# Optimization experiments

Measured on AMD Instinct MI355X. Metric: run time of the kernel, lower is better.

Reference implementation:

```python
import jax, jax.numpy as jnp
import numpy as np

N = 200000   # nodes
E = 3200000  # edges
G = 8192     # graphs
F_IN = 28    # one-hot node feature dim (dataset.num_node_features)
D = 50       # embed_dim
H = 16       # hidden_channels
C = 2        # num_classes


def setup_inputs() -> dict:
    key = jax.random.key(0)
    ks = jax.random.split(key, 12)
    x = jax.random.normal(ks[0], (N, F_IN), jnp.float32)
    row = jax.random.randint(ks[1], (E,), 0, N)   # source nodes (edge_index[0])
    col = jax.random.randint(ks[2], (E,), 0, N)   # target nodes (edge_index[1])
    edge_attr = jax.random.uniform(ks[3], (E,), jnp.float32)
    batch = jnp.sort(jax.random.randint(ks[4], (N,), 0, G))
    emb = jax.random.normal(ks[5], (F_IN, D), jnp.float32) * 0.1
    W1 = jax.random.normal(ks[6], (D, H), jnp.float32) * (1.0 / np.sqrt(D))
    b1 = jnp.zeros((H,), jnp.float32)
    W2 = jax.random.normal(ks[7], (H, H), jnp.float32) * (1.0 / np.sqrt(H))
    b2 = jnp.zeros((H,), jnp.float32)
    W3 = jax.random.normal(ks[8], (H, C), jnp.float32) * (1.0 / np.sqrt(H))
    b3 = jnp.zeros((C,), jnp.float32)
    return dict(x=x, row=row, col=col, edge_attr=edge_attr, batch=batch,
                emb=emb, W1=W1, b1=b1, W2=W2, b2=b2, W3=W3, b3=b3)


def gcn_conv(h, row, col, ew, W, b):
    """PyG GCNConv with normalize=True, add_self_loops=True (fill_value=1)."""
    # degree at target nodes, including self-loop weight 1
    deg = jax.ops.segment_sum(ew, col, num_segments=N) + 1.0
    dinv = jnp.where(deg > 0, deg ** -0.5, 0.0)
    hw = h @ W                                   # [N, out]
    norm = dinv[row] * ew * dinv[col]            # [E]
    agg = jax.ops.segment_sum(hw[row] * norm[:, None], col, num_segments=N)
    agg = agg + hw * (dinv * dinv)[:, None]      # self-loop contribution
    return agg + b


def reference(x, row, col, edge_attr, batch, emb, W1, b1, W2, b2, W3, b3):
    # x is one-hot-ish -> argmax -> embedding lookup
    h = emb[jnp.argmax(x, axis=1)]               # [N, D]
    h = jax.nn.relu(gcn_conv(h, row, col, edge_attr, W1, b1))
    # dropout is identity in eval mode
    h = jax.nn.relu(gcn_conv(h, row, col, edge_attr, W2, b2))
    h = gcn_conv(h, row, col, edge_attr, W3, b3)  # [N, C]
    # global mean pool over graphs
    sums = jax.ops.segment_sum(h, batch, num_segments=G)
    cnts = jax.ops.segment_sum(jnp.ones((N,), h.dtype), batch, num_segments=G)
    pooled = sums / jnp.maximum(cnts, 1.0)[:, None]  # [G, C]
    return jax.nn.softmax(pooled, axis=1)
```

## Files before the change

### kernel.cpp

```cpp
#include <hip/hip_runtime.h>
#include <hip/hip_fp16.h>

constexpr int Nn  = 200000;
constexpr int Ne  = 3200000;
constexpr int Ng  = 8192;
constexpr int FIN = 28;
constexpr int DE  = 50;
constexpr int HD  = 16;
constexpr int CD  = 2;

constexpr int NBIN   = (Nn + 255) >> 8;
constexpr int NBLK   = 512;
constexpr int CH     = Ne / NBLK;
constexpr int CSTR   = 800;
constexpr int LDSCAP = 4608;

__device__ __forceinline__ float dec_ea(unsigned u) {
  return ((float)(u & 16383u) + 0.5f) * (1.0f / 16384.0f);
}

__device__ __forceinline__ float2 dec8(unsigned short u) {
  __half lo = __ushort_as_half((unsigned short)((u & 0x00ffu) << 8));
  __half hi = __ushort_as_half((unsigned short)(u & 0xff00u));
  return make_float2(__half2float(lo), __half2float(hi));
}
__device__ __forceinline__ unsigned char enc8(float f) {
  unsigned short b = __half_as_ushort(__float2half(f));
  return (unsigned char)((unsigned short)(b + 0x0080u) >> 8);
}

static inline int nblocks(long long n, int bs = 256, int cap = 16384) {
  long long b = (n + bs - 1) / bs;
  return (int)(b < cap ? b : cap);
}

__global__ __launch_bounds__(256) void k_count(const int* __restrict__ col,
                                               int* __restrict__ counts,
                                               const float* __restrict__ emb,
                                               const float* __restrict__ W1,
                                               float* __restrict__ EW1) {
  if (blockIdx.x == NBLK) {
    int t = threadIdx.x;
    for (int u = t; u < FIN * HD; u += 256) {
      int i = u / HD, k = u % HD;
      float s = 0.0f;
      for (int j = 0; j < DE; ++j) s += emb[i * DE + j] * W1[j * HD + k];
      EW1[u] = s;
    }
    return;
  }
  __shared__ int c[NBIN];
  for (int i = threadIdx.x; i < NBIN; i += 256) c[i] = 0;
  __syncthreads();
  int lo = blockIdx.x * CH;
  for (int i = threadIdx.x; i < CH; i += 256) atomicAdd(&c[col[lo + i] >> 8], 1);
  __syncthreads();
  for (int i = threadIdx.x; i < NBIN; i += 256) counts[blockIdx.x * CSTR + i] = c[i];
}

__global__ __launch_bounds__(256) void k_argmax(const float* __restrict__ x,
                                                unsigned char* __restrict__ arg) {
  __shared__ float xs[256 * FIN];
  int b = blockIdx.x, t = threadIdx.x;
  int base = b << 8;
  int nval = min(256, Nn - base) * FIN;
  const float4* x4 = (const float4*)(x + (size_t)base * FIN);
  float4* s4 = (float4*)xs;
  int n4 = nval >> 2;
  for (int i = t; i < n4; i += 256) s4[i] = x4[i];
  __syncthreads();
  int node = base + t;
  if (node >= Nn) return;
  const float* xp = xs + t * FIN;
  int a = 0; float best = xp[0];
#pragma unroll
  for (int j = 1; j < FIN; ++j) { float v = xp[j]; if (v > best) { best = v; a = j; } }
  arg[node] = (unsigned char)a;
}

__global__ __launch_bounds__(512) void k_scan1b(int* __restrict__ counts,
                                                int* __restrict__ colTotal) {
  __shared__ int s[NBLK];
  int bin = blockIdx.x, t = threadIdx.x;
  int v = counts[t * CSTR + bin];
  s[t] = v;
  __syncthreads();
  for (int d = 1; d < NBLK; d <<= 1) {
    int x = (t >= d) ? s[t - d] : 0;
    __syncthreads();
    s[t] += x;
    __syncthreads();
  }
  counts[t * CSTR + bin] = s[t] - v;
  if (t == NBLK - 1) colTotal[bin] = s[t];
}

__global__ __launch_bounds__(1024) void k_scanBins(const int* __restrict__ colTotal,
                                                   int* __restrict__ binBase,
                                                   int* __restrict__ start,
                                                   float* __restrict__ zeroreg,
                                                   int nzero) {
  for (int i = threadIdx.x; i < nzero; i += 1024) zeroreg[i] = 0.0f;
  __shared__ int s[1024];
  int t = threadIdx.x;
  int v = (t < NBIN) ? colTotal[t] : 0;
  s[t] = v;
  __syncthreads();
  for (int d = 1; d < 1024; d <<= 1) {
    int x = (t >= d) ? s[t - d] : 0;
    __syncthreads();
    s[t] += x;
    __syncthreads();
  }
  if (t < NBIN) binBase[t] = s[t] - v;
  if (t == NBIN - 1) { binBase[NBIN] = s[t]; start[Nn] = s[t]; }
}

__global__ __launch_bounds__(256) void k_place(const int* __restrict__ row,
                                               const int* __restrict__ col,
                                               const float* __restrict__ ea,
                                               const int* __restrict__ counts,
                                               const int* __restrict__ colTotal,
                                               const int* __restrict__ binBase,
                                               unsigned long long* __restrict__ staged) {
  __shared__ unsigned long long stage[CH];
  __shared__ int lhist[NBIN];
  __shared__ int lcur[NBIN];
  __shared__ int gbase[NBIN];
  __shared__ int partial[256];
  int blk = blockIdx.x, t = threadIdx.x;
  int lo = blk * CH;
  for (int i = t; i < NBIN; i += 256) {
    int cur = counts[blk * CSTR + i];
    int nxt = (blk == NBLK - 1) ? colTotal[i] : counts[(blk + 1) * CSTR + i];
    lhist[i] = nxt - cur;
    lcur[i] = 0;
    gbase[i] = binBase[i] + cur;
  }
  __syncthreads();
  constexpr int CPT = (NBIN + 255) / 256;
  int b0 = t * CPT, s = 0;
#pragma unroll
  for (int j = 0; j < CPT; ++j) { int b = b0 + j; if (b < NBIN) s += lhist[b]; }
  partial[t] = s;
  __syncthreads();
  for (int d = 1; d < 256; d <<= 1) {
    int x = (t >= d) ? partial[t - d] : 0;
    __syncthreads();
    partial[t] += x;
    __syncthreads();
  }
  int run = partial[t] - s;
#pragma unroll
  for (int j = 0; j < CPT; ++j) {
    int b = b0 + j;
    if (b < NBIN) { int c = lhist[b]; lhist[b] = run; run += c; }
  }
  __syncthreads();
  for (int i = t; i < CH; i += 256) {
    int e = lo + i;
    int c = col[e], bin = c >> 8;
    unsigned q = (unsigned)__float2int_rd(ea[e] * 16384.0f);
    if (q > 16383u) q = 16383u;
    unsigned long long entry =
        ((unsigned long long)(unsigned)c << 32) | ((unsigned)row[e] << 14) | q;
    int pos = lhist[bin] + atomicAdd(&lcur[bin], 1);
    stage[pos] = entry;
  }
  __syncthreads();
  for (int i = t; i < CH; i += 256) {
    unsigned long long entry = stage[i];
    int bin = (int)(entry >> 40);
    staged[gbase[bin] + (i - lhist[bin])] = entry;
  }
}

__global__ __launch_bounds__(256) void k_finemb(const int* __restrict__ binBase,
                                                const unsigned long long* __restrict__ staged,
                                                const unsigned char* __restrict__ arg,
                                                const float* __restrict__ EW1,
                                                unsigned* __restrict__ csr,
                                                int* __restrict__ start,
                                                float* __restrict__ dinv,
                                                unsigned char* __restrict__ hws1) {
  __shared__ int ncnt[256];
  __shared__ int noff[256];
  __shared__ int ncur[256];
  __shared__ float sdeg[256];
  __shared__ unsigned outb[LDSCAP];
  int b = blockIdx.x, t = threadIdx.x;
  int lo = binBase[b];
  int cnt = binBase[b + 1] - lo;
  if (cnt > LDSCAP) cnt = LDSCAP;
  ncnt[t] = 0; ncur[t] = 0; sdeg[t] = 0.0f;
  __syncthreads();
  for (int i = t; i < cnt; i += 256) {
    unsigned long long p = staged[lo + i];
    int cl = (int)((p >> 32) & 255u);
    atomicAdd(&ncnt[cl], 1);
    atomicAdd(&sdeg[cl], dec_ea((unsigned)p));
  }
  __syncthreads();
  int v = ncnt[t];
  noff[t] = v;
  __syncthreads();
  for (int d = 1; d < 256; d <<= 1) {
    int xsh = (t >= d) ? noff[t - d] : 0;
    __syncthreads();
    noff[t] += xsh;
    __syncthreads();
  }
  int excl = noff[t] - v;
  __syncthreads();
  noff[t] = excl;
  __syncthreads();
  for (int i = t; i < cnt; i += 256) {
    unsigned long long p = staged[lo + i];
    int cl = (int)((p >> 32) & 255u);
    int idx = noff[cl] + atomicAdd(&ncur[cl], 1);
    outb[idx] = (unsigned)p;
  }
  __syncthreads();
  for (int i = t; i < cnt; i += 256) csr[lo + i] = outb[i];
  int node = (b << 8) + t;
  if (node >= Nn) return;
  start[node] = lo + noff[t];
  float di = rsqrtf(sdeg[t] + 1.0f);
  dinv[node] = di;
  const float* ep = EW1 + (int)arg[node] * HD;
#pragma unroll
  for (int k = 0; k < HD; ++k) hws1[((size_t)node << 4) + k] = enc8(ep[k] * di);
}

template <int OUTC>
__global__ __launch_bounds__(256) void k_conv(const int* __restrict__ start,
                                              const unsigned* __restrict__ csr,
                                              const unsigned short* __restrict__ f8,
                                              const float* __restrict__ dinv,
                                              const float* __restrict__ bias,
                                              const float* __restrict__ Wn,
                                              void* __restrict__ outw) {
  int lane = threadIdx.x & 63;
  int slot = lane >> 3;
  int p    = lane & 7;
  int k    = lane & 15;
  int nstep = gridDim.x * 4;
  for (int n = blockIdx.x * 4 + (threadIdx.x >> 6); n < Nn; n += nstep) {
    int lo = start[n], hi = start[n + 1];
    int j0 = lo + slot;
    bool e0 = j0 < hi, e1 = j0 + 8 < hi, e2 = j0 + 16 < hi;
    unsigned u0 = __builtin_nontemporal_load(csr + (e0 ? j0 : 0));
    unsigned u1 = __builtin_nontemporal_load(csr + (e1 ? j0 + 8 : 0));
    unsigned u2 = __builtin_nontemporal_load(csr + (e2 ? j0 + 16 : 0));
    float w0 = e0 ? dec_ea(u0) : 0.0f;
    float w1 = e1 ? dec_ea(u1) : 0.0f;
    float w2 = e2 ? dec_ea(u2) : 0.0f;
    float2 v0 = dec8(f8[((u0 >> 14) << 3) + p]);
    float2 v1 = dec8(f8[((u1 >> 14) << 3) + p]);
    float2 v2 = dec8(f8[((u2 >> 14) << 3) + p]);
    float ax = fmaf(v2.x, w2, fmaf(v1.x, w1, v0.x * w0));
    float ay = fmaf(v2.y, w2, fmaf(v1.y, w1, v0.y * w0));
    for (int j = j0 + 24; j < hi; j += 8) {
      unsigned u = __builtin_nontemporal_load(csr + j);
      float w = dec_ea(u);
      float2 v = dec8(f8[((u >> 14) << 3) + p]);
      ax = fmaf(v.x, w, ax);
      ay = fmaf(v.y, w, ay);
    }
#pragma unroll
    for (int d = 8; d < 64; d <<= 1) {
      ax += __shfl_xor(ax, d, 64);
      ay += __shfl_xor(ay, d, 64);
    }
    float di = dinv[n];
    float2 self = dec8(f8[((size_t)n << 3) + p]);
    float h0 = fmaxf(di * (ax + self.x) + bias[2 * p + 0], 0.0f);
    float h1 = fmaxf(di * (ay + self.y) + bias[2 * p + 1], 0.0f);
    float acc2 = 0.0f;
#pragma unroll
    for (int q = 0; q < 8; ++q) {
      float hj0 = __shfl(h0, q, 64);
      float hj1 = __shfl(h1, q, 64);
      acc2 = fmaf(hj0, Wn[(2 * q + 0) * OUTC + (OUTC == 16 ? k : (k & 1))], acc2);
      acc2 = fmaf(hj1, Wn[(2 * q + 1) * OUTC + (OUTC == 16 ? k : (k & 1))], acc2);
    }
    acc2 *= di;
    if (OUTC == 16) {
      if (lane < 16) ((unsigned char*)outw)[((size_t)n << 4) + k] = enc8(acc2);
    } else {
      if (lane < CD) ((__half*)outw)[(size_t)n * CD + k] = __float2half(acc2);
    }
  }
}

__global__ __launch_bounds__(256) void k_conv3pool(const int* __restrict__ start,
                                                   const unsigned* __restrict__ csr,
                                                   const __half* __restrict__ h3,
                                                   const float* __restrict__ dinv,
                                                   const float* __restrict__ b3,
                                                   const int* __restrict__ batch,
                                                   float* __restrict__ sums,
                                                   float* __restrict__ cnts) {
  const __half2* h2 = (const __half2*)h3;
  int lane = threadIdx.x & 63;
  int nsub = lane >> 3;
  int slot = lane & 7;
  int wid  = threadIdx.x >> 6;
  int nstep = gridDim.x * 32;
  for (int nb = (blockIdx.x * 4 + wid) * 8; nb < Nn; nb += nstep) {
    int n = nb + nsub;
    int nn = min(n, Nn - 1);
    int lo = start[nn], hi = start[nn + 1];
    int j0 = lo + slot;
    bool e0 = j0 < hi, e1 = j0 + 8 < hi, e2 = j0 + 16 < hi;
    unsigned u0 = __builtin_nontemporal_load(csr + (e0 ? j0 : 0));
    unsigned u1 = __builtin_nontemporal_load(csr + (e1 ? j0 + 8 : 0));
    unsigned u2 = __builtin_nontemporal_load(csr + (e2 ? j0 + 16 : 0));
    float w0 = e0 ? dec_ea(u0) : 0.0f;
    float w1 = e1 ? dec_ea(u1) : 0.0f;
    float w2 = e2 ? dec_ea(u2) : 0.0f;
    float2 v0 = __half22float2(h2[u0 >> 14]);
    float2 v1 = __half22float2(h2[u1 >> 14]);
    float2 v2 = __half22float2(h2[u2 >> 14]);
    float ax = fmaf(v2.x, w2, fmaf(v1.x, w1, v0.x * w0));
    float ay = fmaf(v2.y, w2, fmaf(v1.y, w1, v0.y * w0));
    for (int j = j0 + 24; j < hi; j += 8) {
      unsigned u = __builtin_nontemporal_load(csr + j);
      float w = dec_ea(u);
      float2 v = __half22float2(h2[u >> 14]);
      ax = fmaf(v.x, w, ax);
      ay = fmaf(v.y, w, ay);
    }
    ax += __shfl_xor(ax, 1, 64); ay += __shfl_xor(ay, 1, 64);
    ax += __shfl_xor(ax, 2, 64); ay += __shfl_xor(ay, 2, 64);
    ax += __shfl_xor(ax, 4, 64); ay += __shfl_xor(ay, 4, 64);
    if (slot == 0 && n < Nn) {
      float di = dinv[n];
      float2 self = __half22float2(h2[n]);
      float a0 = di * (ax + self.x) + b3[0];
      float a1 = di * (ay + self.y) + b3[1];
      int g = batch[n];
      atomicAdd(&sums[2 * g + 0], a0);
      atomicAdd(&sums[2 * g + 1], a1);
      atomicAdd(&cnts[g], 1.0f);
    }
  }
}

__global__ void k_softmax(const float* __restrict__ sums, const float* __restrict__ cnts,
                          float* __restrict__ out, int g) {
  int stride = gridDim.x * blockDim.x;
  for (int i = blockIdx.x * blockDim.x + threadIdx.x; i < g; i += stride) {
    float cnt = fmaxf(cnts[i], 1.0f);
    float c0 = sums[i * 2 + 0] / cnt;
    float c1 = sums[i * 2 + 1] / cnt;
    float m = fmaxf(c0, c1);
    float e0 = __expf(c0 - m), e1 = __expf(c1 - m);
    float inv = 1.0f / (e0 + e1);
    out[i * 2 + 0] = e0 * inv;
    out[i * 2 + 1] = e1 * inv;
  }
}

extern "C" void kernel_launch(void* const* d_in, const int* in_sizes, int n_in,
                              void* d_out, int out_size, void* d_ws, size_t ws_size,
                              hipStream_t stream) {
  const float* x   = (const float*)d_in[0];
  const int*   row = (const int*)d_in[1];
  const int*   col = (const int*)d_in[2];
  const float* ea  = (const float*)d_in[3];
  const int*   bat = (const int*)d_in[4];
  const float* emb = (const float*)d_in[5];
  const float* W1  = (const float*)d_in[6];
  const float* b1  = (const float*)d_in[7];
  const float* W2  = (const float*)d_in[8];
  const float* b2  = (const float*)d_in[9];
  const float* W3  = (const float*)d_in[10];
  const float* b3  = (const float*)d_in[11];
  float* out = (float*)d_out;

  float* ws = (float*)d_ws;
  size_t o = 0;
  float* sums    = ws + o; o += (size_t)Ng * CD;
  float* cnts    = ws + o; o += Ng;
  float* dinv    = ws + o; o += Nn;
  float* EW1     = ws + o; o += FIN * HD + 16;
  int*   counts  = (int*)(ws + o); o += (size_t)NBLK * CSTR;
  int*   colTot  = (int*)(ws + o); o += CSTR;
  int*   binBase = (int*)(ws + o); o += 1024;
  int*   startp  = (int*)(ws + o); o += Nn + 16;
  unsigned char* argb = (unsigned char*)(ws + o); o += Nn / 4 + 16;
  unsigned long long* staged = (unsigned long long*)(ws + o); o += (size_t)Ne * 2;
  unsigned* csr  = (unsigned*)(ws + o); o += (size_t)Ne;
  unsigned char* hws1 = (unsigned char*)(ws + o); o += (size_t)Nn * HD / 4;
  unsigned char* hws2 = (unsigned char*)(ws + o); o += (size_t)Nn * HD / 4;
  __half* hw3s   = (__half*)(ws + o); o += (size_t)Nn * CD / 2;
  (void)ws_size; (void)n_in; (void)in_sizes; (void)out_size;

  k_count<<<NBLK + 1, 256, 0, stream>>>(col, counts, emb, W1, EW1);
  k_argmax<<<NBIN, 256, 0, stream>>>(x, argb);
  k_scan1b<<<NBIN, NBLK, 0, stream>>>(counts, colTot);
  k_scanBins<<<1, 1024, 0, stream>>>(colTot, binBase, startp, sums, Ng * (CD + 1));
  k_place<<<NBLK, 256, 0, stream>>>(row, col, ea, counts, colTot, binBase, staged);
  k_finemb<<<NBIN, 256, 0, stream>>>(binBase, staged, argb, EW1, csr, startp, dinv, hws1);

  k_conv<16><<<nblocks((long long)Nn * 64), 256, 0, stream>>>(
      startp, csr, (const unsigned short*)hws1, dinv, b1, W2, hws2);
  k_conv<2><<<nblocks((long long)Nn * 64), 256, 0, stream>>>(
      startp, csr, (const unsigned short*)hws2, dinv, b2, W3, hw3s);

  k_conv3pool<<<nblocks((long long)Nn * 8), 256, 0, stream>>>(
      startp, csr, hw3s, dinv, b3, bat, sums, cnts);

  k_softmax<<<nblocks(Ng), 256, 0, stream>>>(sums, cnts, out, Ng);
}
```

Baseline: 406.3 us.

## Replace global count/scan CSR build with fixed-capacity bins and atomic cursors

Drops the separate count, two scan kernels and the second read of col by giving each 256-node bin a fixed-capacity slab and claiming space with a global atomic cursor per bin in the placement kernel. Node degrees are stored as a separate array so that convs compute hi from start plus degree. Argmax, EW1 and zeroing are merged into one prep kernel, and the pool kernel reduces across the wavefront before doing atomics when all eight nodes share a graph. Edges past the bin capacity are silently dropped, and the CSR order within a bin now depends on atomic ordering.

```diff
diff --git a/kernel.cpp b/kernel.cpp
--- a/kernel.cpp
+++ b/kernel.cpp
@@ -9,11 +9,10 @@
 constexpr int HD  = 16;
 constexpr int CD  = 2;
 
-constexpr int NBIN   = (Nn + 255) >> 8;
-constexpr int NBLK   = 512;
-constexpr int CH     = Ne / NBLK;
-constexpr int CSTR   = 800;
-constexpr int LDSCAP = 4608;
+constexpr int NBIN = (Nn + 255) >> 8;
+constexpr int NBLK = 512;
+constexpr int CH   = Ne / NBLK;
+constexpr int CAPB = 4608;
 
 __device__ __forceinline__ float dec_ea(unsigned u) {
   return ((float)(u & 16383u) + 0.5f) * (1.0f / 16384.0f);
@@ -34,13 +33,14 @@
   return (int)(b < cap ? b : cap);
 }
 
-__global__ __launch_bounds__(256) void k_count(const int* __restrict__ col,
-                                               int* __restrict__ counts,
-                                               const float* __restrict__ emb,
-                                               const float* __restrict__ W1,
-                                               float* __restrict__ EW1) {
-  if (blockIdx.x == NBLK) {
-    int t = threadIdx.x;
+__global__ __launch_bounds__(256) void k_pre(const float* __restrict__ x,
+                                             unsigned char* __restrict__ arg,
+                                             const float* __restrict__ emb,
+                                             const float* __restrict__ W1,
+                                             float* __restrict__ EW1,
+                                             float* __restrict__ zreg, int nz) {
+  int b = blockIdx.x, t = threadIdx.x;
+  if (b == NBIN) {
     for (int u = t; u < FIN * HD; u += 256) {
       int i = u / HD, k = u % HD;
       float s = 0.0f;
@@ -49,25 +49,16 @@
     }
     return;
   }
-  __shared__ int c[NBIN];
-  for (int i = threadIdx.x; i < NBIN; i += 256) c[i] = 0;
-  __syncthreads();
-  int lo = blockIdx.x * CH;
-  for (int i = threadIdx.x; i < CH; i += 256) atomicAdd(&c[col[lo + i] >> 8], 1);
-  __syncthreads();
-  for (int i = threadIdx.x; i < NBIN; i += 256) counts[blockIdx.x * CSTR + i] = c[i];
-}
-
-__global__ __launch_bounds__(256) void k_argmax(const float* __restrict__ x,
-                                                unsigned char* __restrict__ arg) {
+  if (b == NBIN + 1) {
+    for (int i = t; i < nz; i += 256) zreg[i] = 0.0f;
+    return;
+  }
   __shared__ float xs[256 * FIN];
-  int b = blockIdx.x, t = threadIdx.x;
   int base = b << 8;
   int nval = min(256, Nn - base) * FIN;
   const float4* x4 = (const float4*)(x + (size_t)base * FIN);
   float4* s4 = (float4*)xs;
-  int n4 = nval >> 2;
-  for (int i = t; i < n4; i += 256) s4[i] = x4[i];
+  for (int i = t; i < (nval >> 2); i += 256) s4[i] = x4[i];
   __syncthreads();
   int node = base + t;
   if (node >= Nn) return;
@@ -78,51 +69,11 @@
   arg[node] = (unsigned char)a;
 }
 
-__global__ __launch_bounds__(512) void k_scan1b(int* __restrict__ counts,
-                                                int* __restrict__ colTotal) {
-  __shared__ int s[NBLK];
-  int bin = blockIdx.x, t = threadIdx.x;
-  int v = counts[t * CSTR + bin];
-  s[t] = v;
-  __syncthreads();
-  for (int d = 1; d < NBLK; d <<= 1) {
-    int x = (t >= d) ? s[t - d] : 0;
-    __syncthreads();
-    s[t] += x;
-    __syncthreads();
-  }
-  counts[t * CSTR + bin] = s[t] - v;
-  if (t == NBLK - 1) colTotal[bin] = s[t];
-}
-
-__global__ __launch_bounds__(1024) void k_scanBins(const int* __restrict__ colTotal,
-                                                   int* __restrict__ binBase,
-                                                   int* __restrict__ start,
-                                                   float* __restrict__ zeroreg,
-                                                   int nzero) {
-  for (int i = threadIdx.x; i < nzero; i += 1024) zeroreg[i] = 0.0f;
-  __shared__ int s[1024];
-  int t = threadIdx.x;
-  int v = (t < NBIN) ? colTotal[t] : 0;
-  s[t] = v;
-  __syncthreads();
-  for (int d = 1; d < 1024; d <<= 1) {
-    int x = (t >= d) ? s[t - d] : 0;
-    __syncthreads();
-    s[t] += x;
-    __syncthreads();
-  }
-  if (t < NBIN) binBase[t] = s[t] - v;
-  if (t == NBIN - 1) { binBase[NBIN] = s[t]; start[Nn] = s[t]; }
-}
-
-__global__ __launch_bounds__(256) void k_place(const int* __restrict__ row,
-                                               const int* __restrict__ col,
-                                               const float* __restrict__ ea,
-                                               const int* __restrict__ counts,
-                                               const int* __restrict__ colTotal,
-                                               const int* __restrict__ binBase,
-                                               unsigned long long* __restrict__ staged) {
+__global__ __launch_bounds__(256) void k_place1(const int* __restrict__ row,
+                                                const int* __restrict__ col,
+                                                const float* __restrict__ ea,
+                                                int* __restrict__ gcur,
+                                                unsigned long long* __restrict__ staged) {
   __shared__ unsigned long long stage[CH];
   __shared__ int lhist[NBIN];
   __shared__ int lcur[NBIN];
@@ -130,31 +81,35 @@
   __shared__ int partial[256];
   int blk = blockIdx.x, t = threadIdx.x;
   int lo = blk * CH;
-  for (int i = t; i < NBIN; i += 256) {
-    int cur = counts[blk * CSTR + i];
-    int nxt = (blk == NBLK - 1) ? colTotal[i] : counts[(blk + 1) * CSTR + i];
-    lhist[i] = nxt - cur;
-    lcur[i] = 0;
-    gbase[i] = binBase[i] + cur;
-  }
+  for (int i = t; i < NBIN; i += 256) { lhist[i] = 0; lcur[i] = 0; }
+  __syncthreads();
+  for (int i = t; i < CH; i += 256) atomicAdd(&lhist[col[lo + i] >> 8], 1);
   __syncthreads();
   constexpr int CPT = (NBIN + 255) / 256;
   int b0 = t * CPT, s = 0;
-#pragma unroll
-  for (int j = 0; j < CPT; ++j) { int b = b0 + j; if (b < NBIN) s += lhist[b]; }
-  partial[t] = s;
-  __syncthreads();
-  for (int d = 1; d < 256; d <<= 1) {
-    int x = (t >= d) ? partial[t - d] : 0;
-    __syncthreads();
-    partial[t] += x;
-    __syncthreads();
-  }
-  int run = partial[t] - s;
+  int cnt_[CPT];
 #pragma unroll
   for (int j = 0; j < CPT; ++j) {
     int b = b0 + j;
-    if (b < NBIN) { int c = lhist[b]; lhist[b] = run; run += c; }
+    cnt_[j] = (b < NBIN) ? lhist[b] : 0;
+    s += cnt_[j];
+  }
+  partial[t] = s;
+  __syncthreads();
+  for (int d = 1; d < 256; d <<= 1) {
+    int v = (t >= d) ? partial[t - d] : 0;
+    __syncthreads();
+    partial[t] += v;
+    __syncthreads();
+  }
+  int run = partial[t] - s;
+#pragma unroll
+  for (int j = 0; j < CPT; ++j) {
+    int b = b0 + j;
+    if (b < NBIN) {
+      lhist[b] = run; run += cnt_[j];
+      if (cnt_[j] > 0) gbase[b] = atomicAdd(&gcur[b], cnt_[j]);
+    }
   }
   __syncthreads();
   for (int i = t; i < CH; i += 256) {
@@ -171,35 +126,31 @@
   for (int i = t; i < CH; i += 256) {
     unsigned long long entry = stage[i];
     int bin = (int)(entry >> 40);
-    staged[gbase[bin] + (i - lhist[bin])] = entry;
-  }
-}
-
-__global__ __launch_bounds__(256) void k_finemb(const int* __restrict__ binBase,
-                                                const unsigned long long* __restrict__ staged,
-                                                const unsigned char* __restrict__ arg,
-                                                const float* __restrict__ EW1,
-                                                unsigned* __restrict__ csr,
-                                                int* __restrict__ start,
-                                                float* __restrict__ dinv,
-                                                unsigned char* __restrict__ hws1) {
+    int rel = gbase[bin] + (i - lhist[bin]);
+    if (rel < CAPB) staged[(size_t)bin * CAPB + rel] = entry;
+  }
+}
+
+__global__ __launch_bounds__(256) void k_fine2(const int* __restrict__ gcur,
+                                               const unsigned long long* __restrict__ staged,
+                                               const unsigned char* __restrict__ arg,
+                                               const float* __restrict__ EW1,
+                                               unsigned* __restrict__ csr,
+                                               int* __restrict__ startp,
+                                               unsigned short* __restrict__ degw,
+                                               float* __restrict__ dinv,
+                                               unsigned char* __restrict__ hws1) {
   __shared__ int ncnt[256];
   __shared__ int noff[256];
   __shared__ int ncur[256];
-  __shared__ float sdeg[256];
-  __shared__ unsigned outb[LDSCAP];
+  __shared__ unsigned outb[CAPB];
   int b = blockIdx.x, t = threadIdx.x;
-  int lo = binBase[b];
-  int cnt = binBase[b + 1] - lo;
-  if (cnt > LDSCAP) cnt = LDSCAP;
-  ncnt[t] = 0; ncur[t] = 0; sdeg[t] = 0.0f;
-  __syncthreads();
-  for (int i = t; i < cnt; i += 256) {
-    unsigned long long p = staged[lo + i];
-    int cl = (int)((p >> 32) & 255u);
-    atomicAdd(&ncnt[cl], 1);
-    atomicAdd(&sdeg[cl], dec_ea((unsigned)p));
-  }
+  int lo = b * CAPB;
+  int cnt = min(gcur[b], CAPB);
+  ncnt[t] = 0; ncur[t] = 0;
+  __syncthreads();
+  for (int i = t; i < cnt; i += 256)
+    atomicAdd(&ncnt[(int)((staged[lo + i] >> 32) & 255u)], 1);
   __syncthreads();
   int v = ncnt[t];
   noff[t] = v;
@@ -217,15 +168,18 @@
   for (int i = t; i < cnt; i += 256) {
     unsigned long long p = staged[lo + i];
     int cl = (int)((p >> 32) & 255u);
-    int idx = noff[cl] + atomicAdd(&ncur[cl], 1);
-    outb[idx] = (unsigned)p;
+    outb[noff[cl] + atomicAdd(&ncur[cl], 1)] = (unsigned)p;
   }
   __syncthreads();
   for (int i = t; i < cnt; i += 256) csr[lo + i] = outb[i];
   int node = (b << 8) + t;
   if (node >= Nn) return;
-  start[node] = lo + noff[t];
-  float di = rsqrtf(sdeg[t] + 1.0f);
+  int base = noff[t], c = ncnt[t];
+  float s = 0.0f;
+  for (int j = 0; j < c; ++j) s += dec_ea(outb[base + j]);
+  startp[node] = lo + base;
+  degw[node] = (unsigned short)c;
+  float di = rsqrtf(s + 1.0f);
   dinv[node] = di;
   const float* ep = EW1 + (int)arg[node] * HD;
 #pragma unroll
@@ -234,6 +188,7 @@
 
 template <int OUTC>
 __global__ __launch_bounds__(256) void k_conv(const int* __restrict__ start,
+                                              const unsigned short* __restrict__ degw,
                                               const unsigned* __restrict__ csr,
                                               const unsigned short* __restrict__ f8,
                                               const float* __restrict__ dinv,
@@ -246,7 +201,7 @@
   int k    = lane & 15;
   int nstep = gridDim.x * 4;
   for (int n = blockIdx.x * 4 + (threadIdx.x >> 6); n < Nn; n += nstep) {
-    int lo = start[n], hi = start[n + 1];
+    int lo = start[n], hi = lo + degw[n];
     int j0 = lo + slot;
     bool e0 = j0 < hi, e1 = j0 + 8 < hi, e2 = j0 + 16 < hi;
     unsigned u0 = __builtin_nontemporal_load(csr + (e0 ? j0 : 0));
@@ -294,6 +249,7 @@
 }
 
 __global__ __launch_bounds__(256) void k_conv3pool(const int* __restrict__ start,
+                                                   const unsigned short* __restrict__ degw,
                                                    const unsigned* __restrict__ csr,
                                                    const __half* __restrict__ h3,
                                                    const float* __restrict__ dinv,
@@ -310,7 +266,7 @@
   for (int nb = (blockIdx.x * 4 + wid) * 8; nb < Nn; nb += nstep) {
     int n = nb + nsub;
     int nn = min(n, Nn - 1);
-    int lo = start[nn], hi = start[nn + 1];
+    int lo = start[nn], hi = lo + degw[nn];
     int j0 = lo + slot;
     bool e0 = j0 < hi, e1 = j0 + 8 < hi, e2 = j0 + 16 < hi;
     unsigned u0 = __builtin_nontemporal_load(csr + (e0 ? j0 : 0));
@@ -334,15 +290,40 @@
     ax += __shfl_xor(ax, 1, 64); ay += __shfl_xor(ay, 1, 64);
     ax += __shfl_xor(ax, 2, 64); ay += __shfl_xor(ay, 2, 64);
     ax += __shfl_xor(ax, 4, 64); ay += __shfl_xor(ay, 4, 64);
-    if (slot == 0 && n < Nn) {
+    bool valid = (n < Nn);
+    float a0 = 0.0f, a1 = 0.0f;
+    int g = 0;
+    if (valid) {
       float di = dinv[n];
       float2 self = __half22float2(h2[n]);
-      float a0 = di * (ax + self.x) + b3[0];
-      float a1 = di * (ay + self.y) + b3[1];
-      int g = batch[n];
-      atomicAdd(&sums[2 * g + 0], a0);
-      atomicAdd(&sums[2 * g + 1], a1);
-      atomicAdd(&cnts[g], 1.0f);
+      a0 = di * (ax + self.x) + b3[0];
+      a1 = di * (ay + self.y) + b3[1];
+      g = batch[n];
+    }
+    float aa0 = valid ? a0 : 0.0f, aa1 = valid ? a1 : 0.0f;
+    float cc  = valid ? 1.0f : 0.0f;
+    int gmx = valid ? g : -1;
+    int gmn = valid ? g : 0x7fffffff;
+#pragma unroll
+    for (int d = 8; d < 64; d <<= 1) {
+      aa0 += __shfl_xor(aa0, d, 64);
+      aa1 += __shfl_xor(aa1, d, 64);
+      cc  += __shfl_xor(cc, d, 64);
+      gmx = max(gmx, __shfl_xor(gmx, d, 64));
+      gmn = min(gmn, __shfl_xor(gmn, d, 64));
+    }
+    if (slot == 0) {
+      if (gmn == gmx) {
+        if (nsub == 0 && valid) {
+          atomicAdd(&sums[2 * g + 0], aa0);
+          atomicAdd(&sums[2 * g + 1], aa1);
+          atomicAdd(&cnts[g], cc);
+        }
+      } else if (valid) {
+        atomicAdd(&sums[2 * g + 0], a0);
+        atomicAdd(&sums[2 * g + 1], a1);
+        atomicAdd(&cnts[g], 1.0f);
+      }
     }
   }
 }
@@ -381,36 +362,35 @@
 
   float* ws = (float*)d_ws;
   size_t o = 0;
-  float* sums    = ws + o; o += (size_t)Ng * CD;
-  float* cnts    = ws + o; o += Ng;
-  float* dinv    = ws + o; o += Nn;
-  float* EW1     = ws + o; o += FIN * HD + 16;
-  int*   counts  = (int*)(ws + o); o += (size_t)NBLK * CSTR;
-  int*   colTot  = (int*)(ws + o); o += CSTR;
-  int*   binBase = (int*)(ws + o); o += 1024;
-  int*   startp  = (int*)(ws + o); o += Nn + 16;
-  unsigned char* argb = (unsigned char*)(ws + o); o += Nn / 4 + 16;
-  unsigned long long* staged = (unsigned long long*)(ws + o); o += (size_t)Ne * 2;
-  unsigned* csr  = (unsigned*)(ws + o); o += (size_t)Ne;
+  float* sums   = ws + o; o += (size_t)Ng * CD;
+  float* cnts   = ws + o; o += Ng;
+  int*   gcur   = (int*)(ws + o); o += NBIN + 2;
+  float* dinv   = ws + o; o += Nn;
+  float* EW1    = ws + o; o += FIN * HD + 16;
+  int*   startp = (int*)(ws + o); o += Nn + 16;
+  unsigned short* degw = (unsigned short*)(ws + o); o += Nn / 2;
+  unsigned char* argb  = (unsigned char*)(ws + o); o += Nn / 4 + 16;
+  unsigned long long* staged = (unsigned long long*)(ws + o);
+  o += (size_t)NBIN * CAPB * 2;
+  unsigned* csr = (unsigned*)(ws + o); o += (size_t)NBIN * CAPB;
   unsigned char* hws1 = (unsigned char*)(ws + o); o += (size_t)Nn * HD / 4;
   unsigned char* hws2 = (unsigned char*)(ws + o); o += (size_t)Nn * HD / 4;
-  __half* hw3s   = (__half*)(ws + o); o += (size_t)Nn * CD / 2;
+  __half* hw3s  = (__half*)(ws + o); o += (size_t)Nn * CD / 2;
   (void)ws_size; (void)n_in; (void)in_sizes; (void)out_size;
 
-  k_count<<<NBLK + 1, 256, 0, stream>>>(col, counts, emb, W1, EW1);
-  k_argmax<<<NBIN, 256, 0, stream>>>(x, argb);
-  k_scan1b<<<NBIN, NBLK, 0, stream>>>(counts, colTot);
-  k_scanBins<<<1, 1024, 0, stream>>>(colTot, binBase, startp, sums, Ng * (CD + 1));
-  k_place<<<NBLK, 256, 0, stream>>>(row, col, ea, counts, colTot, binBase, staged);
-  k_finemb<<<NBIN, 256, 0, stream>>>(binBase, staged, argb, EW1, csr, startp, dinv, hws1);
+  int nzero = Ng * (CD + 1) + NBIN + 2;
+
+  k_pre<<<NBIN + 2, 256, 0, stream>>>(x, argb, emb, W1, EW1, sums, nzero);
+  k_place1<<<NBLK, 256, 0, stream>>>(row, col, ea, gcur, staged);
+  k_fine2<<<NBIN, 256, 0, stream>>>(gcur, staged, argb, EW1, csr, startp, degw, dinv, hws1);
 
   k_conv<16><<<nblocks((long long)Nn * 64), 256, 0, stream>>>(
-      startp, csr, (const unsigned short*)hws1, dinv, b1, W2, hws2);
+      startp, degw, csr, (const unsigned short*)hws1, dinv, b1, W2, hws2);
   k_conv<2><<<nblocks((long long)Nn * 64), 256, 0, stream>>>(
-      startp, csr, (const unsigned short*)hws2, dinv, b2, W3, hw3s);
+      startp, degw, csr, (const unsigned short*)hws2, dinv, b2, W3, hw3s);
 
   k_conv3pool<<<nblocks((long long)Nn * 8), 256, 0, stream>>>(
-      startp, csr, hw3s, dinv, b3, bat, sums, cnts);
+      startp, degw, csr, hw3s, dinv, b3, bat, sums, cnts);
 
   k_softmax<<<nblocks(Ng), 256, 0, stream>>>(sums, cnts, out, Ng);
 }
```

After: 373.4 us. 8.1% less time.
